# Performance work log

Measured on AMD Instinct MI355X. Metric: run time of the kernel, lower is better.

Reference implementation:

```python
import jax, jax.numpy as jnp
import numpy as np
import math

IN_C = 1024
OUT_C = 1024
HEADS = 16
GROUPS = 4

def grouped_linear(src, weight, bias):
    # src: [..., in_c]; weight: [g, in_c//g, out_c//g]; bias: [out_c]
    g, icg, ocg = weight.shape
    lead = src.shape[:-1]
    s = src.reshape(*lead, g, icg)
    out = jnp.einsum('...gi,gio->...go', s, weight)
    out = out.reshape(*lead, g * ocg)
    return out + bias

def restricted_softmax(src, margin=0.0):
    src_max = jnp.maximum(jnp.max(src, axis=-1, keepdims=True), 0.0)
    out = jnp.exp(src - src_max)
    return out / (jnp.sum(out, axis=-1, keepdims=True) + jnp.exp(margin - src_max))

def setup_inputs() -> dict:
    key = jax.random.key(0)
    ks = jax.random.split(key, 9)
    B, S = 2, 2048
    icg, ocg = IN_C // GROUPS, OUT_C // GROUPS
    scale = 1.0 / math.sqrt(icg)
    return {
        'query': jax.random.normal(ks[0], (B, S, IN_C), jnp.float32),
        'key': jax.random.normal(ks[1], (B, S, IN_C), jnp.float32),
        'value': jax.random.normal(ks[2], (B, S, IN_C), jnp.float32),
        'wq': jax.random.uniform(ks[3], (GROUPS, icg, ocg), jnp.float32, -scale, scale),
        'wk': jax.random.uniform(ks[4], (GROUPS, icg, ocg), jnp.float32, -scale, scale),
        'wv': jax.random.uniform(ks[5], (GROUPS, icg, ocg), jnp.float32, -scale, scale),
        'bq': jax.random.uniform(ks[6], (OUT_C,), jnp.float32, -scale, scale),
        'bk': jax.random.uniform(ks[7], (OUT_C,), jnp.float32, -scale, scale),
        'bv': jax.random.uniform(ks[8], (OUT_C,), jnp.float32, -scale, scale),
    }

def reference(query, key, value, wq, wk, wv, bq, bk, bv):
    q = grouped_linear(query, wq, bq)   # [B,S,OUT_C]
    k = grouped_linear(key, wk, bk)
    v = grouped_linear(value, wv, bv)
    B, Sq, _ = q.shape
    Sk = k.shape[-2]
    d = OUT_C // HEADS
    q = q.reshape(B, Sq, HEADS, d).transpose(0, 2, 1, 3)  # [B,H,Sq,d]
    k = k.reshape(B, Sk, HEADS, d).transpose(0, 2, 1, 3)
    v = v.reshape(B, Sk, HEADS, d).transpose(0, 2, 1, 3)
    score = jnp.einsum('bhqd,bhkd->bhqk', q, k) / math.sqrt(d)
    attn = restricted_softmax(score)
    out = jnp.einsum('bhqk,bhkd->bhqd', attn, v)
    out = out.transpose(0, 2, 1, 3).reshape(B, Sq, OUT_C)
    return out
```

## Files before the change

kernel.cpp:

```cpp
#include <hip/hip_runtime.h>
#include <hip/hip_bf16.h>

#define BB 2
#define SS 2048
#define CC 1024
#define HH 16
#define DDIM 64
#define NROWS (BB*SS)

#define QSC 0.18033688011112042f

typedef __attribute__((ext_vector_type(8))) short bf16x8;
typedef __attribute__((ext_vector_type(4))) float f32x4;

__device__ __forceinline__ f32x4 mfma16(bf16x8 a, bf16x8 b, f32x4 c) {
    return __builtin_amdgcn_mfma_f32_16x16x32_bf16(a, b, c, 0, 0, 0);
}

__global__ __launch_bounds__(256) void prep_wt(
    const float* __restrict__ wq, const float* __restrict__ wk,
    const float* __restrict__ wv, __hip_bfloat16* __restrict__ wt)
{
    const float* w = blockIdx.z == 0 ? wq : blockIdx.z == 1 ? wk : wv;
    const int g  = blockIdx.y;
    const int kt = blockIdx.x >> 2;
    const int nt = blockIdx.x & 3;
    __shared__ __hip_bfloat16 Ls[64][72];
    const int t = threadIdx.x;
    #pragma unroll
    for (int j = 0; j < 4; ++j) {
        int f4 = t + j*256;
        int row = f4 >> 4, n0 = (f4 & 15) * 4;
        float4 f = *(const float4*)&w[(size_t)g*65536 + (size_t)(kt*64+row)*256
                                      + nt*64 + n0];
        Ls[n0+0][row] = __float2bfloat16(f.x);
        Ls[n0+1][row] = __float2bfloat16(f.y);
        Ls[n0+2][row] = __float2bfloat16(f.z);
        Ls[n0+3][row] = __float2bfloat16(f.w);
    }
    __syncthreads();
    #pragma unroll
    for (int j = 0; j < 2; ++j) {
        int u = t + j*256;
        int nr = u >> 3, k8 = (u & 7) * 8;
        *(uint4*)&wt[((size_t)(blockIdx.z*4 + g)*256 + nt*64 + nr)*256
                     + kt*64 + k8] = *(const uint4*)&Ls[nr][k8];
    }
}

__global__ __launch_bounds__(256, 3) void proj_mfma(
    const float* __restrict__ qin, const float* __restrict__ kin,
    const float* __restrict__ vin,
    const __hip_bfloat16* __restrict__ wt,
    const float* __restrict__ bq, const float* __restrict__ bk,
    const float* __restrict__ bv,
    __hip_bfloat16* __restrict__ qs, __hip_bfloat16* __restrict__ ks_,
    __hip_bfloat16* __restrict__ vs)
{
    const int z = blockIdx.z;
    const float* src; const float* bias;
    if (z == 0)      { src = qin; bias = bq; }
    else if (z == 1) { src = kin; bias = bk; }
    else             { src = vin; bias = bv; }

    const int hp   = blockIdx.y;
    const int g    = hp >> 1;
    const int col0 = (hp & 1) * 128;
    const int row0 = blockIdx.x * 128;
    const int b    = row0 >> 11;
    const int s0   = row0 & 2047;

    __shared__ char smem[36864];
    auto As = (__hip_bfloat16 (*)[72])smem;
    auto Ws = (__hip_bfloat16 (*)[72])(smem + 18432);

    const int t    = threadIdx.x;
    const int wid  = t >> 6;
    const int lane = t & 63;
    const int l16  = lane & 15;
    const int quad = lane >> 4;

    f32x4 acc[2][8];
    #pragma unroll
    for (int mt = 0; mt < 2; ++mt)
        #pragma unroll
        for (int nt = 0; nt < 8; ++nt) acc[mt][nt] = (f32x4){0.f,0.f,0.f,0.f};

    const __hip_bfloat16* wtz = wt + (size_t)(z*4 + g)*65536;

    for (int kt = 0; kt < 4; ++kt) {
        __syncthreads();
        #pragma unroll
        for (int j = 0; j < 8; ++j) {
            int idx = t + j*256;
            int row = idx >> 4, c4 = (idx & 15) * 4;
            float4 f = *(const float4*)&src[(size_t)(row0 + row)*CC + g*256
                                            + kt*64 + c4];
            union { __hip_bfloat16 hh[4]; uint2 u; } pk;
            pk.hh[0] = __float2bfloat16(f.x); pk.hh[1] = __float2bfloat16(f.y);
            pk.hh[2] = __float2bfloat16(f.z); pk.hh[3] = __float2bfloat16(f.w);
            *(uint2*)&As[row][c4] = pk.u;
        }
        #pragma unroll
        for (int j = 0; j < 4; ++j) {
            int idx = t + j*256;
            int n = idx >> 3, k8 = (idx & 7) * 8;
            *(uint4*)&Ws[n][k8] =
                *(const uint4*)&wtz[(size_t)(col0 + n)*256 + kt*64 + k8];
        }
        __syncthreads();
        #pragma unroll
        for (int kss = 0; kss < 2; ++kss) {
            bf16x8 af[2], wf[8];
            #pragma unroll
            for (int mt = 0; mt < 2; ++mt)
                af[mt] = *(const bf16x8*)&As[wid*32 + mt*16 + l16][kss*32 + quad*8];
            #pragma unroll
            for (int nt = 0; nt < 8; ++nt)
                wf[nt] = *(const bf16x8*)&Ws[nt*16 + l16][kss*32 + quad*8];
            #pragma unroll
            for (int mt = 0; mt < 2; ++mt)
                #pragma unroll
                for (int nt = 0; nt < 8; ++nt)
                    acc[mt][nt] = mfma16(af[mt], wf[nt], acc[mt][nt]);
        }
    }

    float bval[8];
    #pragma unroll
    for (int nt = 0; nt < 8; ++nt) bval[nt] = bias[g*256 + col0 + nt*16 + l16];

    __syncthreads();

    if (z < 2) {
        const float scale = (z == 0) ? QSC : 1.0f;
        auto Ot = (__hip_bfloat16 (*)[136])smem;
        #pragma unroll
        for (int mt = 0; mt < 2; ++mt)
            #pragma unroll
            for (int nt = 0; nt < 8; ++nt)
                #pragma unroll
                for (int r = 0; r < 4; ++r)
                    Ot[wid*32 + mt*16 + quad*4 + r][nt*16 + l16] =
                        __float2bfloat16((acc[mt][nt][r] + bval[nt]) * scale);
        __syncthreads();
        __hip_bfloat16* base = (z == 0) ? qs : ks_;
        #pragma unroll
        for (int j = 0; j < 8; ++j) {
            int f = wid + j*4;
            int hl = f >> 4, t16l = (f >> 1) & 7, kcs = f & 1;
            uint4 v = *(const uint4*)&Ot[t16l*16 + l16][hl*64 + kcs*32 + quad*8];
            int h = hp*2 + hl;
            int t16g = (s0 >> 4) + t16l;
            *(uint4*)&base[((size_t)(b*HH + h) << 17)
                           + ((size_t)(t16g*2 + kcs) << 9) + lane*8] = v;
        }
    } else {
        auto Vl = (__hip_bfloat16 (*)[136])smem;
        #pragma unroll
        for (int mt = 0; mt < 2; ++mt)
            #pragma unroll
            for (int nt = 0; nt < 8; ++nt) {
                union { __hip_bfloat16 hh[4]; uint2 u; } pk;
                #pragma unroll
                for (int r = 0; r < 4; ++r)
                    pk.hh[r] = __float2bfloat16(acc[mt][nt][r] + bval[nt]);
                *(uint2*)&Vl[nt*16 + l16][wid*32 + mt*16 + quad*4] = pk.u;
            }
        __syncthreads();
        const int kc0 = s0 >> 5;
        #pragma unroll
        for (int j = 0; j < 8; ++j) {
            int f = wid + j*4;
            int hl = f >> 4, dt = (f >> 2) & 3, kcl = f & 3;
            uint4 v = *(const uint4*)&Vl[hl*64 + dt*16 + l16][kcl*32 + quad*8];
            int h = hp*2 + hl;
            *(uint4*)&vs[((size_t)(b*HH + h) << 17)
                         + ((size_t)(dt*64 + kc0 + kcl) << 9) + lane*8] = v;
        }
    }
}

__global__ __launch_bounds__(256, 3) void attn_mfma(
    const __hip_bfloat16* __restrict__ qs, const __hip_bfloat16* __restrict__ ks_,
    const __hip_bfloat16* __restrict__ vs, float* __restrict__ out,
    float* __restrict__ U1, float* __restrict__ L0, float* __restrict__ L1)
{
    const int half = blockIdx.x >> 4;
    const int qt   = blockIdx.x & 15;
    const int h    = blockIdx.y;
    const int b    = blockIdx.z;

    __shared__ __hip_bfloat16 Ps[4][32][72];

    const int t    = threadIdx.x;
    const int wid  = t >> 6;
    const int lane = t & 63;
    const int l16  = lane & 15;
    const int quad = lane >> 4;

    const __hip_bfloat16* qb = qs + ((size_t)(b*HH + h) << 17);
    const __hip_bfloat16* kb = ks_ + ((size_t)(b*HH + h) << 17);
    const __hip_bfloat16* vb = vs + ((size_t)(b*HH + h) << 17);

    const bf16x8 onesv = (bf16x8){16256,16256,16256,16256,
                                  16256,16256,16256,16256};

    bf16x8 qf[2][2];
    #pragma unroll
    for (int mt = 0; mt < 2; ++mt)
        #pragma unroll
        for (int kss = 0; kss < 2; ++kss)
            qf[mt][kss] = *(const bf16x8*)(qb +
                ((size_t)((qt*8 + wid*2 + mt)*2 + kss) << 9) + lane*8);

    f32x4 O[2][4];
    f32x4 Lfrag[2];
    #pragma unroll
    for (int mt = 0; mt < 2; ++mt) {
        Lfrag[mt] = (f32x4){0.f,0.f,0.f,0.f};
        #pragma unroll
        for (int dt = 0; dt < 4; ++dt) O[mt][dt] = (f32x4){0.f,0.f,0.f,0.f};
    }

    const int kt0 = half * 16;
    bf16x8 kf[4][2];
    #pragma unroll
    for (int nt = 0; nt < 4; ++nt)
        #pragma unroll
        for (int kss = 0; kss < 2; ++kss)
            kf[nt][kss] = *(const bf16x8*)(kb +
                ((size_t)(kt0*8 + nt*2 + kss) << 9) + lane*8);

    #pragma unroll
    for (int i = 0; i < 16; ++i) {
        const int kt = kt0 + i;

        bf16x8 vf[4][2];
        #pragma unroll
        for (int dt = 0; dt < 4; ++dt)
            #pragma unroll
            for (int kss = 0; kss < 2; ++kss)
                vf[dt][kss] = *(const bf16x8*)(vb +
                    ((size_t)(dt*64 + kt*2 + kss) << 9) + lane*8);

        f32x4 st[4][2];
        #pragma unroll
        for (int nt = 0; nt < 4; ++nt)
            #pragma unroll
            for (int mt = 0; mt < 2; ++mt) {
                f32x4 z = (f32x4){0.f,0.f,0.f,0.f};
                z = mfma16(kf[nt][0], qf[mt][0], z);
                st[nt][mt] = mfma16(kf[nt][1], qf[mt][1], z);
            }

        if (i < 15) {
            #pragma unroll
            for (int nt = 0; nt < 4; ++nt)
                #pragma unroll
                for (int kss = 0; kss < 2; ++kss)
                    kf[nt][kss] = *(const bf16x8*)(kb +
                        ((size_t)((kt+1)*8 + nt*2 + kss) << 9) + lane*8);
        }

        #pragma unroll
        for (int nt = 0; nt < 4; ++nt)
            #pragma unroll
            for (int mt = 0; mt < 2; ++mt) {
                union { __hip_bfloat16 hh[4]; uint2 u; } pk;
                #pragma unroll
                for (int r = 0; r < 4; ++r)
                    pk.hh[r] = __float2bfloat16(
                        __builtin_amdgcn_exp2f(st[nt][mt][r]));
                *(uint2*)&Ps[wid][mt*16 + l16][nt*16 + quad*4] = pk.u;
            }

        bf16x8 pf[2][2];
        #pragma unroll
        for (int mt = 0; mt < 2; ++mt)
            #pragma unroll
            for (int kss = 0; kss < 2; ++kss)
                pf[mt][kss] = *(const bf16x8*)&Ps[wid][mt*16 + l16][kss*32 + quad*8];

        #pragma unroll
        for (int mt = 0; mt < 2; ++mt) {
            Lfrag[mt] = mfma16(onesv, pf[mt][0], Lfrag[mt]);
            Lfrag[mt] = mfma16(onesv, pf[mt][1], Lfrag[mt]);
        }

        #pragma unroll
        for (int dt = 0; dt < 4; ++dt)
            #pragma unroll
            for (int mt = 0; mt < 2; ++mt) {
                O[mt][dt] = mfma16(vf[dt][0], pf[mt][0], O[mt][dt]);
                O[mt][dt] = mfma16(vf[dt][1], pf[mt][1], O[mt][dt]);
            }
    }

    float* dstU = (half == 0) ? out : U1;
    float* dstL = (half == 0) ? L0 : L1;
    const int qrow0 = qt*128 + wid*32;
    #pragma unroll
    for (int mt = 0; mt < 2; ++mt) {
        const size_t row = (size_t)b*SS + qrow0 + mt*16 + l16;
        if (quad == 0) dstL[row*HH + h] = Lfrag[mt][0];
        #pragma unroll
        for (int dt = 0; dt < 4; ++dt) {
            float4 o4;
            o4.x = O[mt][dt][0]; o4.y = O[mt][dt][1];
            o4.z = O[mt][dt][2]; o4.w = O[mt][dt][3];
            *(float4*)&dstU[row*CC + h*DDIM + dt*16 + quad*4] = o4;
        }
    }
}

__global__ __launch_bounds__(256) void combine(
    float* __restrict__ out, const float* __restrict__ U1,
    const float* __restrict__ L0, const float* __restrict__ L1)
{
    const int idx = blockIdx.x*256 + threadIdx.x;
    const int row = idx >> 8;
    const int c4  = (idx & 255) * 4;
    const int h   = c4 >> 6;
    const float inv = 1.0f / (1.0f + L0[row*HH + h] + L1[row*HH + h]);
    float4 a = *(const float4*)&out[(size_t)idx*4];
    float4 u = *(const float4*)&U1[(size_t)idx*4];
    float4 o;
    o.x = (a.x + u.x)*inv; o.y = (a.y + u.y)*inv;
    o.z = (a.z + u.z)*inv; o.w = (a.w + u.w)*inv;
    *(float4*)&out[(size_t)idx*4] = o;
}

extern "C" void kernel_launch(void* const* d_in, const int* in_sizes, int n_in,
                              void* d_out, int out_size, void* d_ws, size_t ws_size,
                              hipStream_t stream) {
    (void)in_sizes; (void)n_in; (void)out_size; (void)ws_size;
    const float* qin = (const float*)d_in[0];
    const float* kin = (const float*)d_in[1];
    const float* vin = (const float*)d_in[2];
    const float* wq  = (const float*)d_in[3];
    const float* wk  = (const float*)d_in[4];
    const float* wv  = (const float*)d_in[5];
    const float* bq  = (const float*)d_in[6];
    const float* bk  = (const float*)d_in[7];
    const float* bv  = (const float*)d_in[8];

    char* w0 = (char*)d_ws;
    __hip_bfloat16* qs = (__hip_bfloat16*)(w0);
    __hip_bfloat16* ks = (__hip_bfloat16*)(w0 + 8388608);
    __hip_bfloat16* vs = (__hip_bfloat16*)(w0 + 16777216);
    __hip_bfloat16* wt = (__hip_bfloat16*)(w0 + 25165824);
    float* U1 = (float*)(w0 + 26738688);
    float* L0 = (float*)(w0 + 43515904);
    float* L1 = (float*)(w0 + 43778048);
    float* out = (float*)d_out;

    prep_wt<<<dim3(16, 4, 3), 256, 0, stream>>>(wq, wk, wv, wt);
    proj_mfma<<<dim3(32, 8, 3), 256, 0, stream>>>(
        qin, kin, vin, wt, bq, bk, bv, qs, ks, vs);
    attn_mfma<<<dim3(32, 16, 2), 256, 0, stream>>>(qs, ks, vs, out, U1, L0, L1);
    combine<<<dim3(4096), 256, 0, stream>>>(out, U1, L0, L1);
}
```

Baseline: 177.1 us.

## Drop split-K attention and combine kernel; normalize in attention epilogue

Removes the two-way key split in the attention kernel, so each block walks the full key sequence and normalizes its output directly, which eliminates the combine kernel and the U1/L0/L1 intermediate buffers. The exp/pack work is split into two halves so the first P fragments can feed MFMAs while the second half is still being computed, and bf16 conversion uses paired conversions. Launch bounds drop to 2 waves-per-EU hints and the grid halves to 512 blocks, which reduces parallelism and occupancy on the 256-CU device. In exchange it saves the extra global traffic and the extra launch.

Result: faster. 166.5 us (-6.0%).

```diff
diff --git a/kernel.cpp b/kernel.cpp
--- a/kernel.cpp
+++ b/kernel.cpp
@@ -181,15 +181,13 @@
     }
 }
 
-__global__ __launch_bounds__(256, 3) void attn_mfma(
+__global__ __launch_bounds__(256, 2) void attn_mfma(
     const __hip_bfloat16* __restrict__ qs, const __hip_bfloat16* __restrict__ ks_,
-    const __hip_bfloat16* __restrict__ vs, float* __restrict__ out,
-    float* __restrict__ U1, float* __restrict__ L0, float* __restrict__ L1)
+    const __hip_bfloat16* __restrict__ vs, float* __restrict__ out)
 {
-    const int half = blockIdx.x >> 4;
-    const int qt   = blockIdx.x & 15;
-    const int h    = blockIdx.y;
-    const int b    = blockIdx.z;
+    const int qt = blockIdx.x;
+    const int h  = blockIdx.y;
+    const int b  = blockIdx.z;
 
     __shared__ __hip_bfloat16 Ps[4][32][72];
 
@@ -223,19 +221,15 @@
         for (int dt = 0; dt < 4; ++dt) O[mt][dt] = (f32x4){0.f,0.f,0.f,0.f};
     }
 
-    const int kt0 = half * 16;
     bf16x8 kf[4][2];
     #pragma unroll
     for (int nt = 0; nt < 4; ++nt)
         #pragma unroll
         for (int kss = 0; kss < 2; ++kss)
             kf[nt][kss] = *(const bf16x8*)(kb +
-                ((size_t)(kt0*8 + nt*2 + kss) << 9) + lane*8);
-
-    #pragma unroll
-    for (int i = 0; i < 16; ++i) {
-        const int kt = kt0 + i;
-
+                ((size_t)(nt*2 + kss) << 9) + lane*8);
+
+    for (int kt = 0; kt < SS/64; ++kt) {
         bf16x8 vf[4][2];
         #pragma unroll
         for (int dt = 0; dt < 4; ++dt)
@@ -254,7 +248,7 @@
                 st[nt][mt] = mfma16(kf[nt][1], qf[mt][1], z);
             }
 
-        if (i < 15) {
+        if (kt + 1 < SS/64) {
             #pragma unroll
             for (int nt = 0; nt < 4; ++nt)
                 #pragma unroll
@@ -264,71 +258,74 @@
         }
 
         #pragma unroll
-        for (int nt = 0; nt < 4; ++nt)
+        for (int nt = 0; nt < 2; ++nt)
             #pragma unroll
             for (int mt = 0; mt < 2; ++mt) {
-                union { __hip_bfloat16 hh[4]; uint2 u; } pk;
-                #pragma unroll
-                for (int r = 0; r < 4; ++r)
-                    pk.hh[r] = __float2bfloat16(
-                        __builtin_amdgcn_exp2f(st[nt][mt][r]));
+                float2 e0, e1;
+                e0.x = __builtin_amdgcn_exp2f(st[nt][mt][0]);
+                e0.y = __builtin_amdgcn_exp2f(st[nt][mt][1]);
+                e1.x = __builtin_amdgcn_exp2f(st[nt][mt][2]);
+                e1.y = __builtin_amdgcn_exp2f(st[nt][mt][3]);
+                union { __hip_bfloat162 h2[2]; uint2 u; } pk;
+                pk.h2[0] = __float22bfloat162_rn(e0);
+                pk.h2[1] = __float22bfloat162_rn(e1);
                 *(uint2*)&Ps[wid][mt*16 + l16][nt*16 + quad*4] = pk.u;
             }
-
-        bf16x8 pf[2][2];
+        bf16x8 pf0[2];
         #pragma unroll
         for (int mt = 0; mt < 2; ++mt)
-            #pragma unroll
-            for (int kss = 0; kss < 2; ++kss)
-                pf[mt][kss] = *(const bf16x8*)&Ps[wid][mt*16 + l16][kss*32 + quad*8];
+            pf0[mt] = *(const bf16x8*)&Ps[wid][mt*16 + l16][quad*8];
+
+        #pragma unroll
+        for (int nt = 2; nt < 4; ++nt)
+            #pragma unroll
+            for (int mt = 0; mt < 2; ++mt) {
+                float2 e0, e1;
+                e0.x = __builtin_amdgcn_exp2f(st[nt][mt][0]);
+                e0.y = __builtin_amdgcn_exp2f(st[nt][mt][1]);
+                e1.x = __builtin_amdgcn_exp2f(st[nt][mt][2]);
+                e1.y = __builtin_amdgcn_exp2f(st[nt][mt][3]);
+                union { __hip_bfloat162 h2[2]; uint2 u; } pk;
+                pk.h2[0] = __float22bfloat162_rn(e0);
+                pk.h2[1] = __float22bfloat162_rn(e1);
+                *(uint2*)&Ps[wid][mt*16 + l16][nt*16 + quad*4] = pk.u;
+            }
+        bf16x8 pf1[2];
+        #pragma unroll
+        for (int mt = 0; mt < 2; ++mt)
+            pf1[mt] = *(const bf16x8*)&Ps[wid][mt*16 + l16][32 + quad*8];
 
         #pragma unroll
         for (int mt = 0; mt < 2; ++mt) {
-            Lfrag[mt] = mfma16(onesv, pf[mt][0], Lfrag[mt]);
-            Lfrag[mt] = mfma16(onesv, pf[mt][1], Lfrag[mt]);
-        }
-
-        #pragma unroll
-        for (int dt = 0; dt < 4; ++dt)
-            #pragma unroll
-            for (int mt = 0; mt < 2; ++mt) {
-                O[mt][dt] = mfma16(vf[dt][0], pf[mt][0], O[mt][dt]);
-                O[mt][dt] = mfma16(vf[dt][1], pf[mt][1], O[mt][dt]);
-            }
-    }
-
-    float* dstU = (half == 0) ? out : U1;
-    float* dstL = (half == 0) ? L0 : L1;
+            Lfrag[mt] = mfma16(onesv, pf0[mt], Lfrag[mt]);
+            #pragma unroll
+            for (int dt = 0; dt < 4; ++dt)
+                O[mt][dt] = mfma16(vf[dt][0], pf0[mt], O[mt][dt]);
+        }
+        #pragma unroll
+        for (int mt = 0; mt < 2; ++mt) {
+            Lfrag[mt] = mfma16(onesv, pf1[mt], Lfrag[mt]);
+            #pragma unroll
+            for (int dt = 0; dt < 4; ++dt)
+                O[mt][dt] = mfma16(vf[dt][1], pf1[mt], O[mt][dt]);
+        }
+    }
+
     const int qrow0 = qt*128 + wid*32;
     #pragma unroll
     for (int mt = 0; mt < 2; ++mt) {
+        const float inv = 1.0f / (1.0f + Lfrag[mt][0]);
         const size_t row = (size_t)b*SS + qrow0 + mt*16 + l16;
-        if (quad == 0) dstL[row*HH + h] = Lfrag[mt][0];
         #pragma unroll
         for (int dt = 0; dt < 4; ++dt) {
             float4 o4;
-            o4.x = O[mt][dt][0]; o4.y = O[mt][dt][1];
-            o4.z = O[mt][dt][2]; o4.w = O[mt][dt][3];
-            *(float4*)&dstU[row*CC + h*DDIM + dt*16 + quad*4] = o4;
-        }
-    }
-}
-
-__global__ __launch_bounds__(256) void combine(
-    float* __restrict__ out, const float* __restrict__ U1,
-    const float* __restrict__ L0, const float* __restrict__ L1)
-{
-    const int idx = blockIdx.x*256 + threadIdx.x;
-    const int row = idx >> 8;
-    const int c4  = (idx & 255) * 4;
-    const int h   = c4 >> 6;
-    const float inv = 1.0f / (1.0f + L0[row*HH + h] + L1[row*HH + h]);
-    float4 a = *(const float4*)&out[(size_t)idx*4];
-    float4 u = *(const float4*)&U1[(size_t)idx*4];
-    float4 o;
-    o.x = (a.x + u.x)*inv; o.y = (a.y + u.y)*inv;
-    o.z = (a.z + u.z)*inv; o.w = (a.w + u.w)*inv;
-    *(float4*)&out[(size_t)idx*4] = o;
+            o4.x = O[mt][dt][0] * inv;
+            o4.y = O[mt][dt][1] * inv;
+            o4.z = O[mt][dt][2] * inv;
+            o4.w = O[mt][dt][3] * inv;
+            *(float4*)&out[row*CC + h*DDIM + dt*16 + quad*4] = o4;
+        }
+    }
 }
 
 extern "C" void kernel_launch(void* const* d_in, const int* in_sizes, int n_in,
@@ -350,14 +347,10 @@
     __hip_bfloat16* ks = (__hip_bfloat16*)(w0 + 8388608);
     __hip_bfloat16* vs = (__hip_bfloat16*)(w0 + 16777216);
     __hip_bfloat16* wt = (__hip_bfloat16*)(w0 + 25165824);
-    float* U1 = (float*)(w0 + 26738688);
-    float* L0 = (float*)(w0 + 43515904);
-    float* L1 = (float*)(w0 + 43778048);
     float* out = (float*)d_out;
 
     prep_wt<<<dim3(16, 4, 3), 256, 0, stream>>>(wq, wk, wv, wt);
     proj_mfma<<<dim3(32, 8, 3), 256, 0, stream>>>(
         qin, kin, vin, wt, bq, bk, bv, qs, ks, vs);
-    attn_mfma<<<dim3(32, 16, 2), 256, 0, stream>>>(qs, ks, vs, out, U1, L0, L1);
-    combine<<<dim3(4096), 256, 0, stream>>>(out, U1, L0, L1);
-}
+    attn_mfma<<<dim3(16, 16, 2), 256, 0, stream>>>(qs, ks, vs, out);
+}
```
